# Kernel tuning notes

Measured on AMD Instinct MI355X. Metric: run time of the kernel, lower is better.

Reference implementation:

```python
import jax, jax.numpy as jnp
import numpy as np

N_NODES = 50000
N_EDGES = 400000
IN_DIM = 512
HID = 512
HID2 = HID // 2
OUT_DIM = 2
NUM_GRAPHS = 500


def setup_inputs() -> dict:
    key = jax.random.key(0)
    ks = jax.random.split(key, 12)
    x = jax.random.normal(ks[0], (N_NODES, IN_DIM), dtype=jnp.float32)
    edge_index = jax.random.randint(ks[1], (2, N_EDGES), 0, N_NODES, dtype=jnp.int64)
    batch = jnp.sort(jax.random.randint(ks[2], (N_NODES,), 0, NUM_GRAPHS, dtype=jnp.int64))
    def lin(k, fan_out, fan_in):
        bound = 1.0 / np.sqrt(fan_in)
        return jax.random.uniform(k, (fan_out, fan_in), jnp.float32, -bound, bound)
    # SAGEConv layer 1: lin_l (on aggregated neighbors, with bias) + lin_r (root)
    W1l = lin(ks[3], HID, IN_DIM)
    b1 = jax.random.uniform(ks[4], (HID,), jnp.float32, -1/np.sqrt(IN_DIM), 1/np.sqrt(IN_DIM))
    W1r = lin(ks[5], HID, IN_DIM)
    # SAGEConv layer 2
    W2l = lin(ks[6], HID2, HID)
    b2 = jax.random.uniform(ks[7], (HID2,), jnp.float32, -1/np.sqrt(HID), 1/np.sqrt(HID))
    W2r = lin(ks[8], HID2, HID)
    # final fc
    Wfc = lin(ks[9], OUT_DIM, HID2)
    bfc = jax.random.uniform(ks[10], (OUT_DIM,), jnp.float32, -1/np.sqrt(HID2), 1/np.sqrt(HID2))
    return {"x": x, "edge_index": edge_index, "batch": batch,
            "W1l": W1l, "b1": b1, "W1r": W1r,
            "W2l": W2l, "b2": b2, "W2r": W2r,
            "Wfc": Wfc, "bfc": bfc}


def _sage_conv(h, src, dst, Wl, bl, Wr):
    # mean-aggregate source features into target nodes, then linear + root term
    n = h.shape[0]
    agg = jax.ops.segment_sum(h[src], dst, num_segments=n)          # [N, d_in]
    deg = jax.ops.segment_sum(jnp.ones(src.shape, h.dtype), dst, num_segments=n)
    agg = agg / jnp.maximum(deg, 1.0)[:, None]
    return agg @ Wl.T + bl + h @ Wr.T


def reference(x, edge_index, batch, W1l, b1, W1r, W2l, b2, W2r, Wfc, bfc):
    src, dst = edge_index[0], edge_index[1]
    h = jax.nn.relu(_sage_conv(x, src, dst, W1l, b1, W1r))
    h = jax.nn.relu(_sage_conv(h, src, dst, W2l, b2, W2r))
    # global mean pool over graph ids
    pooled = jax.ops.segment_sum(h, batch, num_segments=NUM_GRAPHS)  # [G, HID2]
    counts = jax.ops.segment_sum(jnp.ones(batch.shape, h.dtype), batch, num_segments=NUM_GRAPHS)
    pooled = pooled / jnp.maximum(counts, 1.0)[:, None]
    logits = pooled @ Wfc.T + bfc
    return jax.nn.log_softmax(logits, axis=1)
```

## Files before the change

### kernel.cpp

```cpp
#include <hip/hip_runtime.h>
#include <cstdint>

#define N_NODES 50000
#define N_PAD 50048
#define N_EDGES 400000
#define IN_DIM 512
#define HID 512
#define HID2 256
#define NUM_GRAPHS 500
#define SCAN_BLOCKS 196

typedef unsigned short u16;
typedef short s8v __attribute__((ext_vector_type(8)));
typedef float f4v __attribute__((ext_vector_type(4)));
typedef u16 u16x8 __attribute__((ext_vector_type(8)));
typedef u16 u16x4 __attribute__((ext_vector_type(4)));

__device__ __forceinline__ u16 f2bf(float f) {
  union { float f; uint32_t u; } c;
  c.f = f;
  const uint32_t u = c.u;
  return (u16)((u + 0x7fffu + ((u >> 16) & 1u)) >> 16);
}
__device__ __forceinline__ float bf2f(u16 v) {
  union { uint32_t u; float f; } c;
  c.u = ((uint32_t)v) << 16;
  return c.f;
}

__device__ __forceinline__ void gload16(const void* g, void* l) {
  __builtin_amdgcn_global_load_lds(
      (const __attribute__((address_space(1))) void*)(uintptr_t)g,
      (__attribute__((address_space(3))) void*)(uint32_t)(uintptr_t)l, 16, 0, 0);
}

__device__ __forceinline__ int xcd_swizzle(int orig, int nwg) {
  const int q = nwg >> 3, rr = nwg & 7;
  const int xcd = orig & 7, idx = orig >> 3;
  return (xcd < rr ? xcd * (q + 1) : rr * (q + 1) + (xcd - rr) * q) + idx;
}

__global__ __launch_bounds__(256) void cvt_f32_bf16(const float* __restrict__ in,
                                                    u16* __restrict__ out, int n8) {
  const int i = blockIdx.x * 256 + threadIdx.x;
  if (i >= n8) return;
  const float4 a = ((const float4*)in)[2 * i];
  const float4 b = ((const float4*)in)[2 * i + 1];
  u16x8 o;
  o[0] = f2bf(a.x); o[1] = f2bf(a.y); o[2] = f2bf(a.z); o[3] = f2bf(a.w);
  o[4] = f2bf(b.x); o[5] = f2bf(b.y); o[6] = f2bf(b.z); o[7] = f2bf(b.w);
  ((u16x8*)out)[i] = o;
}

__global__ __launch_bounds__(256) void cvt_weights(const float* __restrict__ W1l,
                                                   const float* __restrict__ W1r,
                                                   const float* __restrict__ W2l,
                                                   const float* __restrict__ W2r,
                                                   u16* __restrict__ Wc1,
                                                   u16* __restrict__ Wc2) {
  const int i = blockIdx.x * 256 + threadIdx.x;
  const float* src;
  u16* dstp;
  int l;
  if (i < 32768)      { src = W1l; dstp = Wc1;          l = i; }
  else if (i < 65536) { src = W1r; dstp = Wc1 + 262144; l = i - 32768; }
  else if (i < 81920) { src = W2l; dstp = Wc2;          l = i - 65536; }
  else                { src = W2r; dstp = Wc2 + 131072; l = i - 81920; }
  const float4 a = ((const float4*)src)[2 * l];
  const float4 b = ((const float4*)src)[2 * l + 1];
  u16x8 o;
  o[0] = f2bf(a.x); o[1] = f2bf(a.y); o[2] = f2bf(a.z); o[3] = f2bf(a.w);
  o[4] = f2bf(b.x); o[5] = f2bf(b.y); o[6] = f2bf(b.z); o[7] = f2bf(b.w);
  ((u16x8*)dstp)[l] = o;
}

template <int K, int NXL2, int NXH>
__global__ __launch_bounds__(256) void gemm_mfma(const u16* __restrict__ A,
                                                 const u16* __restrict__ B,
                                                 u16* __restrict__ CT,
                                                 u16* __restrict__ CR,
                                                 int nwg) {
  __shared__ __align__(16) u16 As[2][128 * 32];
  __shared__ __align__(16) u16 Bs[2][128 * 32];
  const int id = xcd_swizzle(blockIdx.x, nwg);
  const int bx = id & ((1 << NXL2) - 1);
  const int by = id >> NXL2;
  const int tid = threadIdx.x;
  const int lane = tid & 63;
  const int wave = tid >> 6;
  const int wr = (wave >> 1) * 64;
  const int wc = (wave & 1) * 64;
  const int fr = lane & 15;
  const int fq = lane >> 4;
  const size_t bm = (size_t)by * 128;
  const size_t bn = (size_t)bx * 128;

  const int r0 = tid >> 2;
  const int c0 = (((tid & 3) ^ ((tid >> 3) & 3)) * 8);
  const u16* gA = A + (bm + r0) * K + c0;
  const u16* gB = B + (bn + r0) * K + c0;
  const size_t rstep = (size_t)64 * K;
  const int lofs = r0 * 32 + (tid & 3) * 8;
  constexpr int nt = K >> 5;

  auto stage = [&](int b, int kt) {
    const int k0 = kt << 5;
    gload16(gA + k0, &As[b][lofs]);
    gload16(gA + rstep + k0, &As[b][lofs + 64 * 32]);
    gload16(gB + k0, &Bs[b][lofs]);
    gload16(gB + rstep + k0, &Bs[b][lofs + 64 * 32]);
  };

  f4v acc[4][4];
#pragma unroll
  for (int m = 0; m < 4; ++m)
#pragma unroll
    for (int n = 0; n < 4; ++n)
      acc[m][n] = f4v{0.f, 0.f, 0.f, 0.f};

  const int kx = (fr >> 1) & 3;
  const int slot8 = (fq ^ kx) * 8;

  stage(0, 0);
  stage(1, 1);
  asm volatile("s_waitcnt vmcnt(4)" ::: "memory");
  __builtin_amdgcn_s_barrier();

  for (int t = 0; t < nt; ++t) {
    const u16* curA = As[t & 1];
    const u16* curB = Bs[t & 1];
    s8v af[4], bf_[4];
#pragma unroll
    for (int m = 0; m < 4; ++m)
      af[m] = *(const s8v*)(curA + (wr + m * 16 + fr) * 32 + slot8);
#pragma unroll
    for (int n = 0; n < 4; ++n)
      bf_[n] = *(const s8v*)(curB + (wc + n * 16 + fr) * 32 + slot8);
#pragma unroll
    for (int m = 0; m < 4; ++m)
#pragma unroll
      for (int n = 0; n < 4; ++n)
        acc[m][n] = __builtin_amdgcn_mfma_f32_16x16x32_bf16(bf_[n], af[m],
                                                            acc[m][n], 0, 0, 0);
    if (t == nt - 1) break;
    __builtin_amdgcn_s_barrier();
    if (t + 2 < nt) {
      stage(t & 1, t + 2);
      asm volatile("s_waitcnt vmcnt(4)" ::: "memory");
    } else {
      asm volatile("s_waitcnt vmcnt(0)" ::: "memory");
    }
    __builtin_amdgcn_s_barrier();
  }

  u16* Cb = (bx < NXH) ? CT : CR;
  constexpr int ldc = NXH * 128;
  const size_t cn0 = (size_t)(bx - (bx >= NXH ? NXH : 0)) * 128 + wc;
#pragma unroll
  for (int m = 0; m < 4; ++m) {
    const size_t row = bm + wr + m * 16 + fr;
#pragma unroll
    for (int n = 0; n < 4; ++n) {
      const size_t col = cn0 + n * 16 + fq * 4;
      u16x4 p;
#pragma unroll
      for (int i = 0; i < 4; ++i) p[i] = f2bf(acc[m][n][i]);
      *(u16x4*)(Cb + row * ldc + col) = p;
    }
  }
}

__global__ void deg_hist(const int* __restrict__ dst, int* __restrict__ degi, int nE) {
  const int e = blockIdx.x * 256 + threadIdx.x;
  if (e < nE) atomicAdd(&degi[dst[e]], 1);
}

__device__ __forceinline__ int block_scan_excl(int v, int* total_out) {
  const int lane = threadIdx.x & 63;
  const int wid = threadIdx.x >> 6;
  int s = v;
#pragma unroll
  for (int off = 1; off < 64; off <<= 1) {
    const int t = __shfl_up(s, off);
    if (lane >= off) s += t;
  }
  __shared__ int wsum[4];
  if (lane == 63) wsum[wid] = s;
  __syncthreads();
  int base = 0;
#pragma unroll
  for (int w = 0; w < 4; ++w)
    if (w < wid) base += wsum[w];
  *total_out = wsum[0] + wsum[1] + wsum[2] + wsum[3];
  return base + s - v;
}

__global__ __launch_bounds__(256) void scan_blocks(const int* __restrict__ degi,
                                                   int* __restrict__ offs,
                                                   int* __restrict__ bsum, int n) {
  const int gid = blockIdx.x * 256 + threadIdx.x;
  const int v = (gid < n) ? degi[gid] : 0;
  int total;
  const int excl = block_scan_excl(v, &total);
  if (gid < n) offs[gid] = excl;
  if (threadIdx.x == 0) bsum[blockIdx.x] = total;
}

__global__ __launch_bounds__(256) void scan_bsums(int* __restrict__ bsum, int nb) {
  const int v = (threadIdx.x < nb) ? bsum[threadIdx.x] : 0;
  int total;
  const int excl = block_scan_excl(v, &total);
  if (threadIdx.x < nb) bsum[threadIdx.x] = excl;
}

__global__ __launch_bounds__(256) void add_base(int* __restrict__ offs,
                                                const int* __restrict__ bsum,
                                                int n, int nE) {
  const int gid = blockIdx.x * 256 + threadIdx.x;
  if (gid < n) offs[gid] += bsum[blockIdx.x];
  if (gid == 0) offs[n] = nE;
}

__global__ void fill_csr(const int* __restrict__ src, const int* __restrict__ dst,
                         const int* __restrict__ offs, int* __restrict__ cursor,
                         int* __restrict__ sorted_src, int nE) {
  const int e = blockIdx.x * 256 + threadIdx.x;
  if (e < nE) {
    const int d = dst[e];
    const int pos = offs[d] + atomicAdd(&cursor[d], 1);
    sorted_src[pos] = src[e];
  }
}

template <int D, int OUTF32>
__global__ __launch_bounds__(256) void gather_combine(
    const u16* __restrict__ t, const u16* __restrict__ r,
    const float* __restrict__ bias, const int* __restrict__ offs,
    const int* __restrict__ ssrc, void* __restrict__ hout) {
  constexpr int LPN = D / 8;
  const int node = (int)((blockIdx.x * 256u + threadIdx.x) / LPN);
  if (node >= N_NODES) return;
  const int o = (int)(threadIdx.x % LPN) * 8;
  const int beg = offs[node], end = offs[node + 1];
  float a[8] = {0.f, 0.f, 0.f, 0.f, 0.f, 0.f, 0.f, 0.f};
  int e = beg;
  for (; e + 7 < end; e += 8) {
    u16x8 v[8];
#pragma unroll
    for (int q = 0; q < 8; ++q)
      v[q] = *(const u16x8*)(t + (size_t)ssrc[e + q] * D + o);
#pragma unroll
    for (int j = 0; j < 8; ++j)
      a[j] += ((bf2f(v[0][j]) + bf2f(v[1][j])) + (bf2f(v[2][j]) + bf2f(v[3][j]))) +
              ((bf2f(v[4][j]) + bf2f(v[5][j])) + (bf2f(v[6][j]) + bf2f(v[7][j])));
  }
  if (e + 3 < end) {
    u16x8 v[4];
#pragma unroll
    for (int q = 0; q < 4; ++q)
      v[q] = *(const u16x8*)(t + (size_t)ssrc[e + q] * D + o);
#pragma unroll
    for (int j = 0; j < 8; ++j)
      a[j] += (bf2f(v[0][j]) + bf2f(v[1][j])) + (bf2f(v[2][j]) + bf2f(v[3][j]));
    e += 4;
  }
  for (; e < end; ++e) {
    const u16x8 v0 = *(const u16x8*)(t + (size_t)ssrc[e] * D + o);
#pragma unroll
    for (int j = 0; j < 8; ++j) a[j] += bf2f(v0[j]);
  }
  const float invd = 1.0f / fmaxf((float)(end - beg), 1.0f);
  const u16x8 rv = *(const u16x8*)(r + (size_t)node * D + o);
  float hv[8];
#pragma unroll
  for (int j = 0; j < 8; ++j)
    hv[j] = fmaxf(fmaf(a[j], invd, bias[o + j] + bf2f(rv[j])), 0.f);
  if (OUTF32) {
    float* hp = (float*)hout + (size_t)node * D + o;
    *(float4*)hp = make_float4(hv[0], hv[1], hv[2], hv[3]);
    *(float4*)(hp + 4) = make_float4(hv[4], hv[5], hv[6], hv[7]);
  } else {
    u16x8 ov;
#pragma unroll
    for (int j = 0; j < 8; ++j) ov[j] = f2bf(hv[j]);
    *(u16x8*)((u16*)hout + (size_t)node * D + o) = ov;
  }
}

__global__ __launch_bounds__(256) void pool_final(const float* __restrict__ h,
                                                  const int* __restrict__ batch,
                                                  const float* __restrict__ Wfc,
                                                  const float* __restrict__ bfc,
                                                  float* __restrict__ out, int nNodes) {
  const int g = blockIdx.x;
  __shared__ int sbeg, send;
  if (threadIdx.x == 0) {
    int lo = 0, hi = nNodes;
    while (lo < hi) { const int mid = (lo + hi) >> 1; if (batch[mid] < g) lo = mid + 1; else hi = mid; }
    sbeg = lo;
    hi = nNodes;
    while (lo < hi) { const int mid = (lo + hi) >> 1; if (batch[mid] < g + 1) lo = mid + 1; else hi = mid; }
    send = lo;
  }
  __syncthreads();
  const int t = threadIdx.x;
  float s = 0.f;
  for (int row = sbeg; row < send; ++row) s += h[(size_t)row * HID2 + t];
  const float cnt = fmaxf((float)(send - sbeg), 1.0f);
  const float p = s / cnt;
  float d0 = p * Wfc[t];
  float d1 = p * Wfc[HID2 + t];
#pragma unroll
  for (int off = 32; off > 0; off >>= 1) {
    d0 += __shfl_down(d0, off);
    d1 += __shfl_down(d1, off);
  }
  __shared__ float r0[4], r1[4];
  const int wid = t >> 6, lane = t & 63;
  if (lane == 0) { r0[wid] = d0; r1[wid] = d1; }
  __syncthreads();
  if (t == 0) {
    const float l0 = r0[0] + r0[1] + r0[2] + r0[3] + bfc[0];
    const float l1 = r1[0] + r1[1] + r1[2] + r1[3] + bfc[1];
    const float m = fmaxf(l0, l1);
    const float lse = m + logf(expf(l0 - m) + expf(l1 - m));
    out[g * 2 + 0] = l0 - lse;
    out[g * 2 + 1] = l1 - lse;
  }
}

extern "C" void kernel_launch(void* const* d_in, const int* in_sizes, int n_in,
                              void* d_out, int out_size, void* d_ws, size_t ws_size,
                              hipStream_t stream) {
  (void)in_sizes; (void)n_in; (void)out_size; (void)ws_size;
  const float* x   = (const float*)d_in[0];
  const int* eidx  = (const int*)d_in[1];
  const int* batch = (const int*)d_in[2];
  const float* W1l = (const float*)d_in[3];
  const float* b1  = (const float*)d_in[4];
  const float* W1r = (const float*)d_in[5];
  const float* W2l = (const float*)d_in[6];
  const float* b2  = (const float*)d_in[7];
  const float* W2r = (const float*)d_in[8];
  const float* Wfc = (const float*)d_in[9];
  const float* bfc = (const float*)d_in[10];
  float* out = (float*)d_out;
  const int* src = eidx;
  const int* dst = eidx + N_EDGES;

  char* ws = (char*)d_ws;
  size_t off = 0;
  auto alloc = [&](size_t bytes) {
    char* p = ws + off;
    off += (bytes + 255) & ~(size_t)255;
    return p;
  };
  u16* bufT = (u16*)alloc((size_t)N_PAD * 512 * 2);
  u16* bufR = (u16*)alloc((size_t)N_PAD * 512 * 2);
  u16* bufX = (u16*)alloc((size_t)N_PAD * 512 * 2);
  u16* h1   = (u16*)alloc((size_t)N_PAD * 512 * 2);
  u16* Wc1  = (u16*)alloc((size_t)1024 * 512 * 2);
  u16* Wc2  = (u16*)alloc((size_t)512 * 512 * 2);
  int* degi   = (int*)alloc((size_t)N_NODES * 4);
  int* cursor = (int*)alloc((size_t)N_NODES * 4);
  int* offs       = (int*)alloc((size_t)(N_NODES + 1) * 4);
  int* sorted_src = (int*)alloc((size_t)N_EDGES * 4);
  int* bsum       = (int*)alloc((size_t)SCAN_BLOCKS * 4);
  float* h2 = (float*)bufX;

  hipMemsetAsync(degi, 0, 200192 + (size_t)N_NODES * 4, stream);
  deg_hist<<<(N_EDGES + 255) / 256, 256, 0, stream>>>(dst, degi, N_EDGES);
  scan_blocks<<<SCAN_BLOCKS, 256, 0, stream>>>(degi, offs, bsum, N_NODES);
  scan_bsums<<<1, 256, 0, stream>>>(bsum, SCAN_BLOCKS);
  add_base<<<SCAN_BLOCKS, 256, 0, stream>>>(offs, bsum, N_NODES, N_EDGES);
  fill_csr<<<(N_EDGES + 255) / 256, 256, 0, stream>>>(src, dst, offs, cursor,
                                                      sorted_src, N_EDGES);

  cvt_f32_bf16<<<(N_NODES * (IN_DIM / 8) + 255) / 256, 256, 0, stream>>>(
      x, bufX, N_NODES * (IN_DIM / 8));
  cvt_weights<<<384, 256, 0, stream>>>(W1l, W1r, W2l, W2r, Wc1, Wc2);

  {
    const int nwg = (N_PAD / 128) * 8;
    gemm_mfma<IN_DIM, 3, 4><<<nwg, 256, 0, stream>>>(bufX, Wc1, bufT, bufR, nwg);
  }
  gather_combine<HID, 0><<<(N_NODES + 3) / 4, 256, 0, stream>>>(
      bufT, bufR, b1, offs, sorted_src, h1);

  {
    const int nwg = (N_PAD / 128) * 4;
    gemm_mfma<HID, 2, 2><<<nwg, 256, 0, stream>>>(h1, Wc2, bufT, bufR, nwg);
  }
  gather_combine<HID2, 1><<<(N_NODES + 7) / 8, 256, 0, stream>>>(
      bufT, bufR, b2, offs, sorted_src, h2);

  pool_final<<<NUM_GRAPHS, 256, 0, stream>>>(h2, batch, Wfc, bfc, out, N_NODES);
}
```

Baseline: 349.9 us.

## Fuse fp32-to-bf16 input conversion into first GEMM A-tile loads; store h2 as bf16

Removes the separate x conversion kernel. The first GEMM now reads fp32 rows of x into registers, converts them to bf16 and writes them to LDS, prefetching two k-steps ahead. This avoids writing and re-reading a 50k x 512 bf16 copy of x. The cost is that the A tile no longer uses the direct global-to-LDS async path, and each of the 8 column-block workgroups rereads the fp32 A rows at twice the bytes. Separately, the layer-2 output is stored as bf16 and the pooling kernel reads bf16, halving that traffic at some precision cost.

New measurement: 389.7 us. 1.11x slower.

```diff
diff --git a/kernel.cpp b/kernel.cpp
--- a/kernel.cpp
+++ b/kernel.cpp
@@ -38,18 +38,6 @@
   const int q = nwg >> 3, rr = nwg & 7;
   const int xcd = orig & 7, idx = orig >> 3;
   return (xcd < rr ? xcd * (q + 1) : rr * (q + 1) + (xcd - rr) * q) + idx;
-}
-
-__global__ __launch_bounds__(256) void cvt_f32_bf16(const float* __restrict__ in,
-                                                    u16* __restrict__ out, int n8) {
-  const int i = blockIdx.x * 256 + threadIdx.x;
-  if (i >= n8) return;
-  const float4 a = ((const float4*)in)[2 * i];
-  const float4 b = ((const float4*)in)[2 * i + 1];
-  u16x8 o;
-  o[0] = f2bf(a.x); o[1] = f2bf(a.y); o[2] = f2bf(a.z); o[3] = f2bf(a.w);
-  o[4] = f2bf(b.x); o[5] = f2bf(b.y); o[6] = f2bf(b.z); o[7] = f2bf(b.w);
-  ((u16x8*)out)[i] = o;
 }
 
 __global__ __launch_bounds__(256) void cvt_weights(const float* __restrict__ W1l,
@@ -74,8 +62,9 @@
   ((u16x8*)dstp)[l] = o;
 }
 
-template <int K, int NXL2, int NXH>
+template <int K, int NXL2, int NXH, int AF32>
 __global__ __launch_bounds__(256) void gemm_mfma(const u16* __restrict__ A,
+                                                 const float* __restrict__ Af,
                                                  const u16* __restrict__ B,
                                                  u16* __restrict__ CT,
                                                  u16* __restrict__ CR,
@@ -96,19 +85,45 @@
   const size_t bn = (size_t)bx * 128;
 
   const int r0 = tid >> 2;
-  const int c0 = (((tid & 3) ^ ((tid >> 3) & 3)) * 8);
-  const u16* gA = A + (bm + r0) * K + c0;
-  const u16* gB = B + (bn + r0) * K + c0;
-  const size_t rstep = (size_t)64 * K;
+  const int cg = ((tid & 3) ^ ((tid >> 3) & 3));
+  const u16* gB = B + (bn + r0) * K + cg * 8;
   const int lofs = r0 * 32 + (tid & 3) * 8;
   constexpr int nt = K >> 5;
 
-  auto stage = [&](int b, int kt) {
+  const u16* gA = nullptr;
+  const float* gAf0 = nullptr;
+  const float* gAf1 = nullptr;
+  size_t rstepA = 0;
+  if (AF32) {
+    const int ar0 = min((int)bm + r0, N_NODES - 1);
+    const int ar1 = min((int)bm + r0 + 64, N_NODES - 1);
+    gAf0 = Af + (size_t)ar0 * K + cg * 8;
+    gAf1 = Af + (size_t)ar1 * K + cg * 8;
+  } else {
+    gA = A + (bm + r0) * K + cg * 8;
+    rstepA = (size_t)64 * K;
+  }
+  const size_t rstepB = (size_t)64 * K;
+
+  auto stageB = [&](int b, int kt) {
+    const int k0 = kt << 5;
+    gload16(gB + k0, &Bs[b][lofs]);
+    gload16(gB + rstepB + k0, &Bs[b][lofs + 64 * 32]);
+  };
+  auto stageA_lds = [&](int b, int kt) {
     const int k0 = kt << 5;
     gload16(gA + k0, &As[b][lofs]);
-    gload16(gA + rstep + k0, &As[b][lofs + 64 * 32]);
-    gload16(gB + k0, &Bs[b][lofs]);
-    gload16(gB + rstep + k0, &Bs[b][lofs + 64 * 32]);
+    gload16(gA + rstepA + k0, &As[b][lofs + 64 * 32]);
+  };
+  auto writeA = [&](int b, const float4& v0, const float4& v1,
+                    const float4& v2, const float4& v3) {
+    u16x8 w0, w1;
+    w0[0] = f2bf(v0.x); w0[1] = f2bf(v0.y); w0[2] = f2bf(v0.z); w0[3] = f2bf(v0.w);
+    w0[4] = f2bf(v1.x); w0[5] = f2bf(v1.y); w0[6] = f2bf(v1.z); w0[7] = f2bf(v1.w);
+    w1[0] = f2bf(v2.x); w1[1] = f2bf(v2.y); w1[2] = f2bf(v2.z); w1[3] = f2bf(v2.w);
+    w1[4] = f2bf(v3.x); w1[5] = f2bf(v3.y); w1[6] = f2bf(v3.z); w1[7] = f2bf(v3.w);
+    *(u16x8*)(&As[b][lofs]) = w0;
+    *(u16x8*)(&As[b][lofs + 64 * 32]) = w1;
   };
 
   f4v acc[4][4];
@@ -121,12 +136,36 @@
   const int kx = (fr >> 1) & 3;
   const int slot8 = (fq ^ kx) * 8;
 
-  stage(0, 0);
-  stage(1, 1);
-  asm volatile("s_waitcnt vmcnt(4)" ::: "memory");
+  if (AF32) {
+    {
+      float4 v0 = *(const float4*)(gAf0 + 0), v1 = *(const float4*)(gAf0 + 4);
+      float4 v2 = *(const float4*)(gAf1 + 0), v3 = *(const float4*)(gAf1 + 4);
+      writeA(0, v0, v1, v2, v3);
+    }
+    stageB(0, 0);
+    {
+      float4 v0 = *(const float4*)(gAf0 + 32), v1 = *(const float4*)(gAf0 + 36);
+      float4 v2 = *(const float4*)(gAf1 + 32), v3 = *(const float4*)(gAf1 + 36);
+      writeA(1, v0, v1, v2, v3);
+    }
+    stageB(1, 1);
+    asm volatile("s_waitcnt lgkmcnt(0)" ::: "memory");
+  } else {
+    stageA_lds(0, 0); stageB(0, 0);
+    stageA_lds(1, 1); stageB(1, 1);
+    asm volatile("s_waitcnt vmcnt(4)" ::: "memory");
+  }
   __builtin_amdgcn_s_barrier();
 
   for (int t = 0; t < nt; ++t) {
+    float4 av0, av1, av2, av3;
+    if (AF32 && t + 2 < nt) {
+      const int k0 = (t + 2) << 5;
+      av0 = *(const float4*)(gAf0 + k0);
+      av1 = *(const float4*)(gAf0 + k0 + 4);
+      av2 = *(const float4*)(gAf1 + k0);
+      av3 = *(const float4*)(gAf1 + k0 + 4);
+    }
     const u16* curA = As[t & 1];
     const u16* curB = Bs[t & 1];
     s8v af[4], bf_[4];
@@ -145,8 +184,15 @@
     if (t == nt - 1) break;
     __builtin_amdgcn_s_barrier();
     if (t + 2 < nt) {
-      stage(t & 1, t + 2);
-      asm volatile("s_waitcnt vmcnt(4)" ::: "memory");
+      if (AF32) {
+        stageB(t & 1, t + 2);
+        writeA(t & 1, av0, av1, av2, av3);
+        asm volatile("s_waitcnt lgkmcnt(0)" ::: "memory");
+      } else {
+        stageA_lds(t & 1, t + 2);
+        stageB(t & 1, t + 2);
+        asm volatile("s_waitcnt vmcnt(4)" ::: "memory");
+      }
     } else {
       asm volatile("s_waitcnt vmcnt(0)" ::: "memory");
     }
@@ -287,7 +333,7 @@
   }
 }
 
-__global__ __launch_bounds__(256) void pool_final(const float* __restrict__ h,
+__global__ __launch_bounds__(256) void pool_final(const u16* __restrict__ h,
                                                   const int* __restrict__ batch,
                                                   const float* __restrict__ Wfc,
                                                   const float* __restrict__ bfc,
@@ -305,7 +351,7 @@
   __syncthreads();
   const int t = threadIdx.x;
   float s = 0.f;
-  for (int row = sbeg; row < send; ++row) s += h[(size_t)row * HID2 + t];
+  for (int row = sbeg; row < send; ++row) s += bf2f(h[(size_t)row * HID2 + t]);
   const float cnt = fmaxf((float)(send - sbeg), 1.0f);
   const float p = s / cnt;
   float d0 = p * Wfc[t];
@@ -357,8 +403,8 @@
   };
   u16* bufT = (u16*)alloc((size_t)N_PAD * 512 * 2);
   u16* bufR = (u16*)alloc((size_t)N_PAD * 512 * 2);
-  u16* bufX = (u16*)alloc((size_t)N_PAD * 512 * 2);
   u16* h1   = (u16*)alloc((size_t)N_PAD * 512 * 2);
+  u16* h2   = (u16*)alloc((size_t)N_NODES * 256 * 2);
   u16* Wc1  = (u16*)alloc((size_t)1024 * 512 * 2);
   u16* Wc2  = (u16*)alloc((size_t)512 * 512 * 2);
   int* degi   = (int*)alloc((size_t)N_NODES * 4);
@@ -366,7 +412,6 @@
   int* offs       = (int*)alloc((size_t)(N_NODES + 1) * 4);
   int* sorted_src = (int*)alloc((size_t)N_EDGES * 4);
   int* bsum       = (int*)alloc((size_t)SCAN_BLOCKS * 4);
-  float* h2 = (float*)bufX;
 
   hipMemsetAsync(degi, 0, 200192 + (size_t)N_NODES * 4, stream);
   deg_hist<<<(N_EDGES + 255) / 256, 256, 0, stream>>>(dst, degi, N_EDGES);
@@ -376,22 +421,22 @@
   fill_csr<<<(N_EDGES + 255) / 256, 256, 0, stream>>>(src, dst, offs, cursor,
                                                       sorted_src, N_EDGES);
 
-  cvt_f32_bf16<<<(N_NODES * (IN_DIM / 8) + 255) / 256, 256, 0, stream>>>(
-      x, bufX, N_NODES * (IN_DIM / 8));
   cvt_weights<<<384, 256, 0, stream>>>(W1l, W1r, W2l, W2r, Wc1, Wc2);
 
   {
     const int nwg = (N_PAD / 128) * 8;
-    gemm_mfma<IN_DIM, 3, 4><<<nwg, 256, 0, stream>>>(bufX, Wc1, bufT, bufR, nwg);
+    gemm_mfma<IN_DIM, 3, 4, 1><<<nwg, 256, 0, stream>>>(nullptr, x, Wc1,
+                                                        bufT, bufR, nwg);
   }
   gather_combine<HID, 0><<<(N_NODES + 3) / 4, 256, 0, stream>>>(
       bufT, bufR, b1, offs, sorted_src, h1);
 
   {
     const int nwg = (N_PAD / 128) * 4;
-    gemm_mfma<HID, 2, 2><<<nwg, 256, 0, stream>>>(h1, Wc2, bufT, bufR, nwg);
-  }
-  gather_combine<HID2, 1><<<(N_NODES + 7) / 8, 256, 0, stream>>>(
+    gemm_mfma<HID, 2, 2, 0><<<nwg, 256, 0, stream>>>(h1, nullptr, Wc2,
+                                                     bufT, bufR, nwg);
+  }
+  gather_combine<HID2, 0><<<(N_NODES + 7) / 8, 256, 0, stream>>>(
       bufT, bufR, b2, offs, sorted_src, h2);
 
   pool_final<<<NUM_GRAPHS, 256, 0, stream>>>(h2, batch, Wfc, bfc, out, N_NODES);
```

## Replace GEMM with 256x256-tile 8-wave pipelined MFMA kernel; store h2 as bf16

Applied to the files above, without the earlier changes.

The 128x128 four-wave GEMM is replaced by a 256x256-tile, 512-thread kernel with K-step 64. It interleaves staged global-to-LDS loads with MFMA phases, uses setprio around the MFMA blocks and puts explicit waitcnt and barriers between phases. The larger tile is meant to raise arithmetic intensity and overlap memory with compute, at the cost of more registers and LDS and fewer workgroups (N_PAD is raised to a multiple of 256). The second-layer output h2 is now written as bf16 rather than fp32, which halves its write and the reads in pooling, at a small precision cost.

New measurement: 370.7 us. 5.9% more time.

```diff
diff --git a/kernel.cpp b/kernel.cpp
--- a/kernel.cpp
+++ b/kernel.cpp
@@ -2,7 +2,7 @@
 #include <cstdint>
 
 #define N_NODES 50000
-#define N_PAD 50048
+#define N_PAD 50176
 #define N_EDGES 400000
 #define IN_DIM 512
 #define HID 512
@@ -74,101 +74,155 @@
   ((u16x8*)dstp)[l] = o;
 }
 
-template <int K, int NXL2, int NXH>
-__global__ __launch_bounds__(256) void gemm_mfma(const u16* __restrict__ A,
-                                                 const u16* __restrict__ B,
-                                                 u16* __restrict__ CT,
-                                                 u16* __restrict__ CR,
-                                                 int nwg) {
-  __shared__ __align__(16) u16 As[2][128 * 32];
-  __shared__ __align__(16) u16 Bs[2][128 * 32];
+#define MFMA16(MH)                                                         \
+  do {                                                                     \
+    __builtin_amdgcn_s_setprio(1);                                         \
+    _Pragma("unroll") for (int m4 = 0; m4 < 4; ++m4) {                     \
+      _Pragma("unroll") for (int n = 0; n < 4; ++n)                        \
+          acc[(MH)*4 + m4][n] = __builtin_amdgcn_mfma_f32_16x16x32_bf16(   \
+              bf[n], af[m4], acc[(MH)*4 + m4][n], 0, 0, 0);                \
+    }                                                                      \
+    __builtin_amdgcn_s_setprio(0);                                         \
+  } while (0)
+
+#define STAGE_A(B2, TT, Q) \
+  gload16(gA + (Q)*64*512 + (TT)*64, &As[B2][(Q)*4096 + ldst])
+#define STAGE_B(B2, TT, KS)                                              \
+  do {                                                                   \
+    gload16(gB + (TT)*64 + (KS)*32, &Bs[B2][(KS)*8192 + ldst]);          \
+    gload16(gB + 128*512 + (TT)*64 + (KS)*32,                            \
+            &Bs[B2][(KS)*8192 + 4096 + ldst]);                           \
+  } while (0)
+
+#define LOAD_AF(B_, KS, MH)                                              \
+  do {                                                                   \
+    const u16* AsQ = &As[B_][(wm*2 + (MH))*4096 + fr*64 +                \
+                            (((((KS) << 2) | fq) ^ frk7) * 8)];          \
+    af[0] = *(const s8v*)(AsQ);                                          \
+    af[1] = *(const s8v*)(AsQ + 1024);                                   \
+    af[2] = *(const s8v*)(AsQ + 2048);                                   \
+    af[3] = *(const s8v*)(AsQ + 3072);                                   \
+  } while (0)
+
+#define LOAD_BF(B_, KS)                                                  \
+  do {                                                                   \
+    const u16* BsS = &Bs[B_][(KS)*8192 + (wn*64 + fr)*32 + bslot];       \
+    bf[0] = *(const s8v*)(BsS);                                          \
+    bf[1] = *(const s8v*)(BsS + 512);                                    \
+    bf[2] = *(const s8v*)(BsS + 1024);                                   \
+    bf[3] = *(const s8v*)(BsS + 1536);                                   \
+  } while (0)
+
+template <int NXBITS, int NXH, int LDC>
+__global__ __launch_bounds__(512) void gemm8p(const u16* __restrict__ A,
+                                              const u16* __restrict__ B,
+                                              u16* __restrict__ CT,
+                                              u16* __restrict__ CR,
+                                              int nwg) {
+  __shared__ __align__(16) u16 As[2][256 * 64];
+  __shared__ __align__(16) u16 Bs[2][2 * 256 * 32];
   const int id = xcd_swizzle(blockIdx.x, nwg);
-  const int bx = id & ((1 << NXL2) - 1);
-  const int by = id >> NXL2;
+  const int bx = id & ((1 << NXBITS) - 1);
+  const int by = id >> NXBITS;
+  const size_t bm = (size_t)by * 256;
+  const size_t bn = (size_t)bx * 256;
   const int tid = threadIdx.x;
   const int lane = tid & 63;
-  const int wave = tid >> 6;
-  const int wr = (wave >> 1) * 64;
-  const int wc = (wave & 1) * 64;
+  const int wv = tid >> 6;
+  const int wm = wv >> 2;
+  const int wn = wv & 3;
   const int fr = lane & 15;
   const int fq = lane >> 4;
-  const size_t bm = (size_t)by * 128;
-  const size_t bn = (size_t)bx * 128;
-
-  const int r0 = tid >> 2;
-  const int c0 = (((tid & 3) ^ ((tid >> 3) & 3)) * 8);
-  const u16* gA = A + (bm + r0) * K + c0;
-  const u16* gB = B + (bn + r0) * K + c0;
-  const size_t rstep = (size_t)64 * K;
-  const int lofs = r0 * 32 + (tid & 3) * 8;
-  constexpr int nt = K >> 5;
-
-  auto stage = [&](int b, int kt) {
-    const int k0 = kt << 5;
-    gload16(gA + k0, &As[b][lofs]);
-    gload16(gA + rstep + k0, &As[b][lofs + 64 * 32]);
-    gload16(gB + k0, &Bs[b][lofs]);
-    gload16(gB + rstep + k0, &Bs[b][lofs + 64 * 32]);
-  };
-
-  f4v acc[4][4];
-#pragma unroll
-  for (int m = 0; m < 4; ++m)
+  const int frk7 = fr & 7;
+  const int bslot = (fq ^ ((fr >> 1) & 3)) * 8;
+
+  const int rA = tid >> 3;
+  const u16* gA = A + (bm + rA) * 512 + ((tid & 7) ^ (rA & 7)) * 8;
+  const int rB = tid >> 2;
+  const u16* gB = B + (bn + rB) * 512 + ((tid & 3) ^ ((rB >> 1) & 3)) * 8;
+  const int ldst = tid * 8;
+
+  f4v acc[8][4];
+#pragma unroll
+  for (int m = 0; m < 8; ++m)
 #pragma unroll
     for (int n = 0; n < 4; ++n)
       acc[m][n] = f4v{0.f, 0.f, 0.f, 0.f};
 
-  const int kx = (fr >> 1) & 3;
-  const int slot8 = (fq ^ kx) * 8;
-
-  stage(0, 0);
-  stage(1, 1);
-  asm volatile("s_waitcnt vmcnt(4)" ::: "memory");
+  STAGE_B(0, 0, 0);
+  STAGE_A(0, 0, 0); STAGE_A(0, 0, 2);
+  STAGE_A(0, 0, 1); STAGE_A(0, 0, 3);
+  STAGE_B(0, 0, 1);
+  asm volatile("s_waitcnt vmcnt(0)" ::: "memory");
   __builtin_amdgcn_s_barrier();
 
-  for (int t = 0; t < nt; ++t) {
-    const u16* curA = As[t & 1];
-    const u16* curB = Bs[t & 1];
-    s8v af[4], bf_[4];
-#pragma unroll
-    for (int m = 0; m < 4; ++m)
-      af[m] = *(const s8v*)(curA + (wr + m * 16 + fr) * 32 + slot8);
-#pragma unroll
-    for (int n = 0; n < 4; ++n)
-      bf_[n] = *(const s8v*)(curB + (wc + n * 16 + fr) * 32 + slot8);
-#pragma unroll
-    for (int m = 0; m < 4; ++m)
-#pragma unroll
-      for (int n = 0; n < 4; ++n)
-        acc[m][n] = __builtin_amdgcn_mfma_f32_16x16x32_bf16(bf_[n], af[m],
-                                                            acc[m][n], 0, 0, 0);
-    if (t == nt - 1) break;
-    __builtin_amdgcn_s_barrier();
-    if (t + 2 < nt) {
-      stage(t & 1, t + 2);
+#pragma unroll 2
+  for (int t = 0; t < 8; ++t) {
+    const int b = t & 1, b2 = b ^ 1;
+    s8v af[4], bf[4];
+    LOAD_AF(b, 0, 0);
+    LOAD_BF(b, 0);
+    if (t < 7) STAGE_B(b2, t + 1, 0);
+    __builtin_amdgcn_s_barrier();
+    asm volatile("s_waitcnt lgkmcnt(0)" ::: "memory");
+    __builtin_amdgcn_sched_barrier(0);
+    MFMA16(0);
+    __builtin_amdgcn_s_barrier();
+    LOAD_AF(b, 0, 1);
+    if (t < 7) {
+      STAGE_A(b2, t + 1, 0); STAGE_A(b2, t + 1, 2);
       asm volatile("s_waitcnt vmcnt(4)" ::: "memory");
     } else {
       asm volatile("s_waitcnt vmcnt(0)" ::: "memory");
     }
     __builtin_amdgcn_s_barrier();
-  }
-
-  u16* Cb = (bx < NXH) ? CT : CR;
-  constexpr int ldc = NXH * 128;
-  const size_t cn0 = (size_t)(bx - (bx >= NXH ? NXH : 0)) * 128 + wc;
-#pragma unroll
-  for (int m = 0; m < 4; ++m) {
-    const size_t row = bm + wr + m * 16 + fr;
+    asm volatile("s_waitcnt lgkmcnt(0)" ::: "memory");
+    __builtin_amdgcn_sched_barrier(0);
+    MFMA16(1);
+    __builtin_amdgcn_s_barrier();
+    LOAD_AF(b, 1, 0);
+    LOAD_BF(b, 1);
+    if (t < 7) { STAGE_A(b2, t + 1, 1); STAGE_A(b2, t + 1, 3); }
+    __builtin_amdgcn_s_barrier();
+    asm volatile("s_waitcnt lgkmcnt(0)" ::: "memory");
+    __builtin_amdgcn_sched_barrier(0);
+    MFMA16(0);
+    __builtin_amdgcn_s_barrier();
+    LOAD_AF(b, 1, 1);
+    if (t < 7) {
+      STAGE_B(b2, t + 1, 1);
+      asm volatile("s_waitcnt vmcnt(2)" ::: "memory");
+    }
+    __builtin_amdgcn_s_barrier();
+    asm volatile("s_waitcnt lgkmcnt(0)" ::: "memory");
+    __builtin_amdgcn_sched_barrier(0);
+    MFMA16(1);
+    __builtin_amdgcn_s_barrier();
+  }
+
+  u16* Cb;
+  size_t cn0;
+  if (bx < NXH) { Cb = CT; cn0 = (size_t)bx * 256; }
+  else          { Cb = CR; cn0 = (size_t)(bx - NXH) * 256; }
+  cn0 += wn * 64;
+#pragma unroll
+  for (int m = 0; m < 8; ++m) {
+    const size_t row = bm + wm * 128 + m * 16 + fr;
 #pragma unroll
     for (int n = 0; n < 4; ++n) {
       const size_t col = cn0 + n * 16 + fq * 4;
       u16x4 p;
 #pragma unroll
       for (int i = 0; i < 4; ++i) p[i] = f2bf(acc[m][n][i]);
-      *(u16x4*)(Cb + row * ldc + col) = p;
+      *(u16x4*)(Cb + row * LDC + col) = p;
     }
   }
 }
+#undef MFMA16
+#undef STAGE_A
+#undef STAGE_B
+#undef LOAD_AF
+#undef LOAD_BF
 
 __global__ void deg_hist(const int* __restrict__ dst, int* __restrict__ degi, int nE) {
   const int e = blockIdx.x * 256 + threadIdx.x;
@@ -287,7 +341,7 @@
   }
 }
 
-__global__ __launch_bounds__(256) void pool_final(const float* __restrict__ h,
+__global__ __launch_bounds__(256) void pool_final(const u16* __restrict__ h,
                                                   const int* __restrict__ batch,
                                                   const float* __restrict__ Wfc,
                                                   const float* __restrict__ bfc,
@@ -305,7 +359,7 @@
   __syncthreads();
   const int t = threadIdx.x;
   float s = 0.f;
-  for (int row = sbeg; row < send; ++row) s += h[(size_t)row * HID2 + t];
+  for (int row = sbeg; row < send; ++row) s += bf2f(h[(size_t)row * HID2 + t]);
   const float cnt = fmaxf((float)(send - sbeg), 1.0f);
   const float p = s / cnt;
   float d0 = p * Wfc[t];
@@ -359,6 +413,7 @@
   u16* bufR = (u16*)alloc((size_t)N_PAD * 512 * 2);
   u16* bufX = (u16*)alloc((size_t)N_PAD * 512 * 2);
   u16* h1   = (u16*)alloc((size_t)N_PAD * 512 * 2);
+  u16* h2   = (u16*)alloc((size_t)N_NODES * 256 * 2);
   u16* Wc1  = (u16*)alloc((size_t)1024 * 512 * 2);
   u16* Wc2  = (u16*)alloc((size_t)512 * 512 * 2);
   int* degi   = (int*)alloc((size_t)N_NODES * 4);
@@ -366,7 +421,6 @@
   int* offs       = (int*)alloc((size_t)(N_NODES + 1) * 4);
   int* sorted_src = (int*)alloc((size_t)N_EDGES * 4);
   int* bsum       = (int*)alloc((size_t)SCAN_BLOCKS * 4);
-  float* h2 = (float*)bufX;
 
   hipMemsetAsync(degi, 0, 200192 + (size_t)N_NODES * 4, stream);
   deg_hist<<<(N_EDGES + 255) / 256, 256, 0, stream>>>(dst, degi, N_EDGES);
@@ -381,17 +435,17 @@
   cvt_weights<<<384, 256, 0, stream>>>(W1l, W1r, W2l, W2r, Wc1, Wc2);
 
   {
-    const int nwg = (N_PAD / 128) * 8;
-    gemm_mfma<IN_DIM, 3, 4><<<nwg, 256, 0, stream>>>(bufX, Wc1, bufT, bufR, nwg);
+    const int nwg = (N_PAD / 256) * 4;
+    gemm8p<2, 2, 512><<<nwg, 512, 0, stream>>>(bufX, Wc1, bufT, bufR, nwg);
   }
   gather_combine<HID, 0><<<(N_NODES + 3) / 4, 256, 0, stream>>>(
       bufT, bufR, b1, offs, sorted_src, h1);
 
   {
-    const int nwg = (N_PAD / 128) * 4;
-    gemm_mfma<HID, 2, 2><<<nwg, 256, 0, stream>>>(h1, Wc2, bufT, bufR, nwg);
-  }
-  gather_combine<HID2, 1><<<(N_NODES + 7) / 8, 256, 0, stream>>>(
+    const int nwg = (N_PAD / 256) * 2;
+    gemm8p<1, 1, 256><<<nwg, 512, 0, stream>>>(h1, Wc2, bufT, bufR, nwg);
+  }
+  gather_combine<HID2, 0><<<(N_NODES + 7) / 8, 256, 0, stream>>>(
       bufT, bufR, b2, offs, sorted_src, h2);
 
   pool_final<<<NUM_GRAPHS, 256, 0, stream>>>(h2, batch, Wfc, bfc, out, N_NODES);
```

## Fuse fp32-to-bf16 input conversion into first GEMM and store h2 as bf16

Applied to the files above, without the earlier changes.

Removes the standalone x conversion kernel. The first GEMM now streams fp32 x tiles directly into LDS with a swizzled layout, then converts them to bf16 with packed cvt instructions before the MFMA. It also writes layer-2 output as bf16 instead of fp32, and the pooling kernel reads bf16. This saves a full read/write pass over x and halves h2 traffic, at the cost of doubled A-tile LDS footprint and global load volume in GEMM1, plus extra conversion ALU work inside the GEMM loop.

After: 357.5 us. +2.2%, slower.

```diff
diff --git a/kernel.cpp b/kernel.cpp
--- a/kernel.cpp
+++ b/kernel.cpp
@@ -27,6 +27,11 @@
   c.u = ((uint32_t)v) << 16;
   return c.f;
 }
+__device__ __forceinline__ uint32_t cvtpk(float lo, float hi) {
+  uint32_t r;
+  asm("v_cvt_pk_bf16_f32 %0, %1, %2" : "=v"(r) : "v"(lo), "v"(hi));
+  return r;
+}
 
 __device__ __forceinline__ void gload16(const void* g, void* l) {
   __builtin_amdgcn_global_load_lds(
@@ -38,18 +43,6 @@
   const int q = nwg >> 3, rr = nwg & 7;
   const int xcd = orig & 7, idx = orig >> 3;
   return (xcd < rr ? xcd * (q + 1) : rr * (q + 1) + (xcd - rr) * q) + idx;
-}
-
-__global__ __launch_bounds__(256) void cvt_f32_bf16(const float* __restrict__ in,
-                                                    u16* __restrict__ out, int n8) {
-  const int i = blockIdx.x * 256 + threadIdx.x;
-  if (i >= n8) return;
-  const float4 a = ((const float4*)in)[2 * i];
-  const float4 b = ((const float4*)in)[2 * i + 1];
-  u16x8 o;
-  o[0] = f2bf(a.x); o[1] = f2bf(a.y); o[2] = f2bf(a.z); o[3] = f2bf(a.w);
-  o[4] = f2bf(b.x); o[5] = f2bf(b.y); o[6] = f2bf(b.z); o[7] = f2bf(b.w);
-  ((u16x8*)out)[i] = o;
 }
 
 __global__ __launch_bounds__(256) void cvt_weights(const float* __restrict__ W1l,
@@ -74,13 +67,15 @@
   ((u16x8*)dstp)[l] = o;
 }
 
-template <int K, int NXL2, int NXH>
+template <int K, int NXL2, int NXH, int AF32>
 __global__ __launch_bounds__(256) void gemm_mfma(const u16* __restrict__ A,
+                                                 const float* __restrict__ Af,
                                                  const u16* __restrict__ B,
                                                  u16* __restrict__ CT,
                                                  u16* __restrict__ CR,
                                                  int nwg) {
-  __shared__ __align__(16) u16 As[2][128 * 32];
+  constexpr int ABYTES = AF32 ? 2 * 128 * 32 * 4 : 2 * 128 * 32 * 2;
+  __shared__ __align__(16) char AsRaw[ABYTES];
   __shared__ __align__(16) u16 Bs[2][128 * 32];
   const int id = xcd_swizzle(blockIdx.x, nwg);
   const int bx = id & ((1 << NXL2) - 1);
@@ -96,20 +91,49 @@
   const size_t bn = (size_t)bx * 128;
 
   const int r0 = tid >> 2;
-  const int c0 = (((tid & 3) ^ ((tid >> 3) & 3)) * 8);
-  const u16* gA = A + (bm + r0) * K + c0;
-  const u16* gB = B + (bn + r0) * K + c0;
-  const size_t rstep = (size_t)64 * K;
-  const int lofs = r0 * 32 + (tid & 3) * 8;
+  const int cgB = ((tid & 3) ^ ((tid >> 3) & 3));
+  const u16* gB = B + (bn + r0) * K + cgB * 8;
+  const int lofsB = r0 * 32 + (tid & 3) * 8;
+  const size_t rstepB = (size_t)64 * K;
   constexpr int nt = K >> 5;
+
+  u16* uAs = (u16*)AsRaw;
+  float* fAs = (float*)AsRaw;
+  const u16* gA = nullptr;
+  const float* gAf0 = nullptr, *gAf1 = nullptr, *gAf2 = nullptr, *gAf3 = nullptr;
+  int lofsA = 0;
+  if (AF32) {
+    const int rA = tid >> 3;
+    const int cA = (tid & 7) ^ (rA & 7);
+    int rr0 = (int)bm + rA;        rr0 = rr0 < N_NODES ? rr0 : N_NODES - 1;
+    int rr1 = (int)bm + rA + 32;   rr1 = rr1 < N_NODES ? rr1 : N_NODES - 1;
+    int rr2 = (int)bm + rA + 64;   rr2 = rr2 < N_NODES ? rr2 : N_NODES - 1;
+    int rr3 = (int)bm + rA + 96;   rr3 = rr3 < N_NODES ? rr3 : N_NODES - 1;
+    gAf0 = Af + (size_t)rr0 * K + cA * 4;
+    gAf1 = Af + (size_t)rr1 * K + cA * 4;
+    gAf2 = Af + (size_t)rr2 * K + cA * 4;
+    gAf3 = Af + (size_t)rr3 * K + cA * 4;
+    lofsA = tid * 4;
+  } else {
+    gA = A + (bm + r0) * K + cgB * 8;
+    lofsA = lofsB;
+  }
 
   auto stage = [&](int b, int kt) {
     const int k0 = kt << 5;
-    gload16(gA + k0, &As[b][lofs]);
-    gload16(gA + rstep + k0, &As[b][lofs + 64 * 32]);
-    gload16(gB + k0, &Bs[b][lofs]);
-    gload16(gB + rstep + k0, &Bs[b][lofs + 64 * 32]);
+    if (AF32) {
+      gload16(gAf0 + k0, &fAs[b * 4096 + lofsA]);
+      gload16(gAf1 + k0, &fAs[b * 4096 + 1024 + lofsA]);
+      gload16(gAf2 + k0, &fAs[b * 4096 + 2048 + lofsA]);
+      gload16(gAf3 + k0, &fAs[b * 4096 + 3072 + lofsA]);
+    } else {
+      gload16(gA + k0, &uAs[b * 4096 + lofsA]);
+      gload16(gA + (size_t)64 * K + k0, &uAs[b * 4096 + 64 * 32 + lofsA]);
+    }
+    gload16(gB + k0, &Bs[b][lofsB]);
+    gload16(gB + rstepB + k0, &Bs[b][lofsB + 64 * 32]);
   };
+  constexpr int NLD = AF32 ? 6 : 4;
 
   f4v acc[4][4];
 #pragma unroll
@@ -118,21 +142,38 @@
     for (int n = 0; n < 4; ++n)
       acc[m][n] = f4v{0.f, 0.f, 0.f, 0.f};
 
+  const int frk = fr & 7;
   const int kx = (fr >> 1) & 3;
   const int slot8 = (fq ^ kx) * 8;
 
   stage(0, 0);
   stage(1, 1);
-  asm volatile("s_waitcnt vmcnt(4)" ::: "memory");
+  if (NLD == 6) asm volatile("s_waitcnt vmcnt(6)" ::: "memory");
+  else          asm volatile("s_waitcnt vmcnt(4)" ::: "memory");
   __builtin_amdgcn_s_barrier();
 
   for (int t = 0; t < nt; ++t) {
-    const u16* curA = As[t & 1];
-    const u16* curB = Bs[t & 1];
+    const int b = t & 1;
     s8v af[4], bf_[4];
-#pragma unroll
-    for (int m = 0; m < 4; ++m)
-      af[m] = *(const s8v*)(curA + (wr + m * 16 + fr) * 32 + slot8);
+    if (AF32) {
+      const float* fA = fAs + b * 4096;
+#pragma unroll
+      for (int m = 0; m < 4; ++m) {
+        const int row = wr + m * 16 + fr;
+        const float4 a0 = *(const float4*)(fA + row * 32 + ((2 * fq) ^ frk) * 4);
+        const float4 a1 = *(const float4*)(fA + row * 32 + ((2 * fq + 1) ^ frk) * 4);
+        union { uint32_t w[4]; s8v v; } u;
+        u.w[0] = cvtpk(a0.x, a0.y); u.w[1] = cvtpk(a0.z, a0.w);
+        u.w[2] = cvtpk(a1.x, a1.y); u.w[3] = cvtpk(a1.z, a1.w);
+        af[m] = u.v;
+      }
+    } else {
+      const u16* curA = uAs + b * 4096;
+#pragma unroll
+      for (int m = 0; m < 4; ++m)
+        af[m] = *(const s8v*)(curA + (wr + m * 16 + fr) * 32 + slot8);
+    }
+    const u16* curB = Bs[b];
 #pragma unroll
     for (int n = 0; n < 4; ++n)
       bf_[n] = *(const s8v*)(curB + (wc + n * 16 + fr) * 32 + slot8);
@@ -145,8 +186,9 @@
     if (t == nt - 1) break;
     __builtin_amdgcn_s_barrier();
     if (t + 2 < nt) {
-      stage(t & 1, t + 2);
-      asm volatile("s_waitcnt vmcnt(4)" ::: "memory");
+      stage(b, t + 2);
+      if (NLD == 6) asm volatile("s_waitcnt vmcnt(6)" ::: "memory");
+      else          asm volatile("s_waitcnt vmcnt(4)" ::: "memory");
     } else {
       asm volatile("s_waitcnt vmcnt(0)" ::: "memory");
     }
@@ -232,11 +274,11 @@
   }
 }
 
-template <int D, int OUTF32>
+template <int D>
 __global__ __launch_bounds__(256) void gather_combine(
     const u16* __restrict__ t, const u16* __restrict__ r,
     const float* __restrict__ bias, const int* __restrict__ offs,
-    const int* __restrict__ ssrc, void* __restrict__ hout) {
+    const int* __restrict__ ssrc, u16* __restrict__ hout) {
   constexpr int LPN = D / 8;
   const int node = (int)((blockIdx.x * 256u + threadIdx.x) / LPN);
   if (node >= N_NODES) return;
@@ -271,23 +313,14 @@
   }
   const float invd = 1.0f / fmaxf((float)(end - beg), 1.0f);
   const u16x8 rv = *(const u16x8*)(r + (size_t)node * D + o);
-  float hv[8];
+  u16x8 ov;
 #pragma unroll
   for (int j = 0; j < 8; ++j)
-    hv[j] = fmaxf(fmaf(a[j], invd, bias[o + j] + bf2f(rv[j])), 0.f);
-  if (OUTF32) {
-    float* hp = (float*)hout + (size_t)node * D + o;
-    *(float4*)hp = make_float4(hv[0], hv[1], hv[2], hv[3]);
-    *(float4*)(hp + 4) = make_float4(hv[4], hv[5], hv[6], hv[7]);
-  } else {
-    u16x8 ov;
-#pragma unroll
-    for (int j = 0; j < 8; ++j) ov[j] = f2bf(hv[j]);
-    *(u16x8*)((u16*)hout + (size_t)node * D + o) = ov;
-  }
-}
-
-__global__ __launch_bounds__(256) void pool_final(const float* __restrict__ h,
+    ov[j] = f2bf(fmaxf(fmaf(a[j], invd, bias[o + j] + bf2f(rv[j])), 0.f));
+  *(u16x8*)(hout + (size_t)node * D + o) = ov;
+}
+
+__global__ __launch_bounds__(256) void pool_final(const u16* __restrict__ h,
                                                   const int* __restrict__ batch,
                                                   const float* __restrict__ Wfc,
                                                   const float* __restrict__ bfc,
@@ -305,7 +338,7 @@
   __syncthreads();
   const int t = threadIdx.x;
   float s = 0.f;
-  for (int row = sbeg; row < send; ++row) s += h[(size_t)row * HID2 + t];
+  for (int row = sbeg; row < send; ++row) s += bf2f(h[(size_t)row * HID2 + t]);
   const float cnt = fmaxf((float)(send - sbeg), 1.0f);
   const float p = s / cnt;
   float d0 = p * Wfc[t];
@@ -357,8 +390,8 @@
   };
   u16* bufT = (u16*)alloc((size_t)N_PAD * 512 * 2);
   u16* bufR = (u16*)alloc((size_t)N_PAD * 512 * 2);
-  u16* bufX = (u16*)alloc((size_t)N_PAD * 512 * 2);
   u16* h1   = (u16*)alloc((size_t)N_PAD * 512 * 2);
+  u16* h2   = (u16*)alloc((size_t)N_NODES * 256 * 2);
   u16* Wc1  = (u16*)alloc((size_t)1024 * 512 * 2);
   u16* Wc2  = (u16*)alloc((size_t)512 * 512 * 2);
   int* degi   = (int*)alloc((size_t)N_NODES * 4);
@@ -366,7 +399,6 @@
   int* offs       = (int*)alloc((size_t)(N_NODES + 1) * 4);
   int* sorted_src = (int*)alloc((size_t)N_EDGES * 4);
   int* bsum       = (int*)alloc((size_t)SCAN_BLOCKS * 4);
-  float* h2 = (float*)bufX;
 
   hipMemsetAsync(degi, 0, 200192 + (size_t)N_NODES * 4, stream);
   deg_hist<<<(N_EDGES + 255) / 256, 256, 0, stream>>>(dst, degi, N_EDGES);
@@ -376,22 +408,22 @@
   fill_csr<<<(N_EDGES + 255) / 256, 256, 0, stream>>>(src, dst, offs, cursor,
                                                       sorted_src, N_EDGES);
 
-  cvt_f32_bf16<<<(N_NODES * (IN_DIM / 8) + 255) / 256, 256, 0, stream>>>(
-      x, bufX, N_NODES * (IN_DIM / 8));
   cvt_weights<<<384, 256, 0, stream>>>(W1l, W1r, W2l, W2r, Wc1, Wc2);
 
   {
     const int nwg = (N_PAD / 128) * 8;
-    gemm_mfma<IN_DIM, 3, 4><<<nwg, 256, 0, stream>>>(bufX, Wc1, bufT, bufR, nwg);
-  }
-  gather_combine<HID, 0><<<(N_NODES + 3) / 4, 256, 0, stream>>>(
+    gemm_mfma<IN_DIM, 3, 4, 1><<<nwg, 256, 0, stream>>>(nullptr, x, Wc1,
+                                                        bufT, bufR, nwg);
+  }
+  gather_combine<HID><<<(N_NODES + 3) / 4, 256, 0, stream>>>(
       bufT, bufR, b1, offs, sorted_src, h1);
 
   {
     const int nwg = (N_PAD / 128) * 4;
-    gemm_mfma<HID, 2, 2><<<nwg, 256, 0, stream>>>(h1, Wc2, bufT, bufR, nwg);
-  }
-  gather_combine<HID2, 1><<<(N_NODES + 7) / 8, 256, 0, stream>>>(
+    gemm_mfma<HID, 2, 2, 0><<<nwg, 256, 0, stream>>>(h1, nullptr, Wc2,
+                                                     bufT, bufR, nwg);
+  }
+  gather_combine<HID2><<<(N_NODES + 7) / 8, 256, 0, stream>>>(
       bufT, bufR, b2, offs, sorted_src, h2);
 
   pool_final<<<NUM_GRAPHS, 256, 0, stream>>>(h2, batch, Wfc, bfc, out, N_NODES);
```
